# Kernel optimization log

Hardware: AMD Instinct MI355X
Metric: run time of the kernel (lower is better)

Reference implementation:

```python
import jax, jax.numpy as jnp
import numpy as np

DIM = 768
HEADS = 12
DIM_HEAD = DIM // HEADS
SEQ = 1024
BATCH = 16
DEPTH = 6
MAX_DEPTH = 12
ALPHA = 0.5


def _decomposed_kernel(n, depth, alpha, max_depth, inverse):
    # symmetric (inverse) matrix square root of the OU-process kernel matrix
    if depth == 0:
        return np.eye(n, dtype=np.float32)
    gamma = -0.5 * np.log(1.0 - alpha ** (2.0 * depth / max_depth))
    ar = np.arange(n, dtype=np.float64)
    K = np.exp(-gamma * np.abs(ar[:, None] - ar[None, :]))
    w, V = np.linalg.eigh(K)
    thr = w.max() * n * np.finfo(w.dtype).eps
    s = np.clip(w, thr, None)
    s = 1.0 / np.sqrt(s) if inverse else np.sqrt(s)
    return ((V * s[None, :]) @ V.T).astype(np.float32)


def _make_buffers():
    prev_inv = _decomposed_kernel(SEQ, DEPTH - 1, ALPHA, MAX_DEPTH, inverse=True)
    cur = _decomposed_kernel(SEQ, DEPTH, ALPHA, MAX_DEPTH, inverse=False)
    A = (cur @ prev_inv).astype(np.float32)
    mn = A.min()
    if mn <= 0:
        A = np.clip(A, abs(mn) + np.finfo(np.float32).eps, None)
    row_sum = A.sum(1)                      # (N,)
    B = np.log(A / row_sum)                 # broadcast over last axis (matches torch)
    d = row_sum.reshape(1, 1, SEQ, 1).astype(np.float32)
    return jnp.asarray(d), jnp.asarray(B[None, None]).astype(jnp.float32)


def setup_inputs() -> dict:
    key = jax.random.key(0)
    kx, kw = jax.random.split(key)
    x = jax.random.normal(kx, (BATCH, SEQ, DIM), dtype=jnp.float32)
    # module zeros the q block; use normal(std=dim^-0.5) everywhere for a non-degenerate test
    w_qkv = jax.random.normal(kw, (3 * DIM, DIM), dtype=jnp.float32) * (DIM ** -0.5)
    b_qkv = jnp.zeros((3 * DIM,), dtype=jnp.float32)
    d, b_bias = _make_buffers()
    return {"x": x, "w_qkv": w_qkv, "b_qkv": b_qkv, "d": d, "b_bias": b_bias}


def reference(x, w_qkv, b_qkv, d, b_bias):
    B, N, D = x.shape
    qkv = x @ w_qkv.T + b_qkv                                   # (B,N,3D)
    qkv = qkv.reshape(B, N, 3, HEADS, DIM_HEAD).transpose(2, 0, 3, 1, 4)
    q, k, v = qkv[0], qkv[1], qkv[2]                            # (B,H,N,dh)
    scale = DIM_HEAD ** -0.5
    scores = jnp.einsum("bhnd,bhmd->bhnm", q, k) * scale + b_bias
    attn = jax.nn.softmax(scores, axis=-1)
    out = d * jnp.einsum("bhnm,bhmd->bhnd", attn, v)            # post-softmax row scale
    return out.transpose(0, 2, 1, 3).reshape(B, N, D)
```

## Files before the change

kernel.cpp:

```cpp
#include <hip/hip_runtime.h>
#include <cstdint>
#include <cstddef>

typedef __attribute__((ext_vector_type(8))) short short8;
typedef __attribute__((ext_vector_type(4))) short short4_;
typedef __attribute__((ext_vector_type(4))) float f32x4;
typedef __attribute__((ext_vector_type(2))) unsigned int uint2_;

__device__ inline unsigned short bf16rne(float f) {
    uint32_t u = __builtin_bit_cast(uint32_t, f);
    u += 0x7fffu + ((u >> 16) & 1u);
    return (unsigned short)(u >> 16);
}

#define GLDS(g, l)                                                              \
    __builtin_amdgcn_global_load_lds(                                           \
        (const __attribute__((address_space(1))) void*)(g),                     \
        (__attribute__((address_space(3))) void*)(l), 16, 0, 0)

__global__ void cvt_kernel(const float* __restrict__ src,
                           unsigned short* __restrict__ dst, int n8) {
    int i = blockIdx.x * blockDim.x + threadIdx.x;
    if (i >= n8) return;
    const float4* s = (const float4*)src + (size_t)i * 2;
    float4 a = s[0], b = s[1];
    uint32_t w0 = bf16rne(a.x) | ((uint32_t)bf16rne(a.y) << 16);
    uint32_t w1 = bf16rne(a.z) | ((uint32_t)bf16rne(a.w) << 16);
    uint32_t w2 = bf16rne(b.x) | ((uint32_t)bf16rne(b.y) << 16);
    uint32_t w3 = bf16rne(b.z) | ((uint32_t)bf16rne(b.w) << 16);
    uint4 o; o.x = w0; o.y = w1; o.z = w2; o.w = w3;
    ((uint4*)dst)[i] = o;
}

__global__ __launch_bounds__(256) void qkv_gemm(
    const unsigned short* __restrict__ X, const unsigned short* __restrict__ W,
    const float* __restrict__ bqkv,
    unsigned short* __restrict__ qo, unsigned short* __restrict__ ko,
    unsigned short* __restrict__ vo)
{
    __shared__ unsigned short smem[16896];
    unsigned short* As = smem;
    unsigned short* Bs = smem + 8192;

    const int tid  = threadIdx.x;
    const int f    = blockIdx.x + gridDim.x * blockIdx.y;
    const int per  = (gridDim.x * gridDim.y) >> 3;
    const int wk   = (f & 7) * per + (f >> 3);
    const int m0   = (wk / 18) * 128;
    const int n0   = (wk % 18) * 128;
    const int wid  = tid >> 6;
    const int lane = tid & 63;
    const int m16  = lane & 15;
    const int quad = lane >> 4;
    const int wm   = wid >> 1, wn = wid & 1;

    f32x4 acc[4][4];
    #pragma unroll
    for (int i = 0; i < 4; i++)
        #pragma unroll
        for (int j = 0; j < 4; j++) acc[i][j] = (f32x4){0.f, 0.f, 0.f, 0.f};

    auto stage = [&](int buf, int k0) {
        #pragma unroll
        for (int rd = 0; rd < 2; ++rd) {
            int id = rd * 256 + tid;
            int row = id >> 2;
            int cs = (id & 3) ^ (row & 3);
            GLDS(X + (size_t)(m0 + row) * 768 + k0 + cs * 8, &As[buf * 4096 + id * 8]);
        }
        #pragma unroll
        for (int rd = 0; rd < 2; ++rd) {
            int id = rd * 256 + tid;
            int row = id >> 2;
            int cs = (id & 3) ^ (row & 3);
            GLDS(W + (size_t)(n0 + row) * 768 + k0 + cs * 8, &Bs[buf * 4096 + id * 8]);
        }
    };

    stage(0, 0);
    __syncthreads();

    const int csw = (quad ^ (m16 & 3)) * 8;
    for (int kt = 0; kt < 24; ++kt) {
        const int cur = kt & 1;
        if (kt < 23) stage(cur ^ 1, (kt + 1) * 32);

        short8 a[4], b[4];
        #pragma unroll
        for (int mb = 0; mb < 4; mb++)
            a[mb] = *(const short8*)&As[cur * 4096 + (wm * 64 + mb * 16 + m16) * 32 + csw];
        #pragma unroll
        for (int nb = 0; nb < 4; nb++)
            b[nb] = *(const short8*)&Bs[cur * 4096 + (wn * 64 + nb * 16 + m16) * 32 + csw];
        __builtin_amdgcn_s_setprio(1);
        #pragma unroll
        for (int mb = 0; mb < 4; mb++)
            #pragma unroll
            for (int nb = 0; nb < 4; nb++)
                acc[mb][nb] = __builtin_amdgcn_mfma_f32_16x16x32_bf16(
                    a[mb], b[nb], acc[mb][nb], 0, 0, 0);
        __builtin_amdgcn_s_setprio(0);
        __syncthreads();
    }

    float bias_n[4];
    #pragma unroll
    for (int nb = 0; nb < 4; nb++) bias_n[nb] = bqkv[n0 + wn * 64 + nb * 16 + m16];

    const int which = n0 / 768;
    const int hbase = (n0 % 768) / 64;
    const int bI  = m0 >> 10;
    const int ns0 = m0 & 1023;

    if (which == 2) {
        #pragma unroll
        for (int mb = 0; mb < 4; ++mb)
            #pragma unroll
            for (int nb = 0; nb < 4; ++nb) {
                int n  = wn * 64 + nb * 16 + m16;
                int hh = hbase + (n >> 6);
                int d  = n & 63;
                int pos = ns0 + wm * 64 + mb * 16 + quad * 4;
                short4_ v4;
                #pragma unroll
                for (int r = 0; r < 4; ++r)
                    v4[r] = (short)bf16rne(acc[mb][nb][r] + bias_n[nb]);
                *(short4_*)(vo + ((size_t)(bI * 12 + hh) * 64 + d) * 1024 + pos) = v4;
            }
        return;
    }

    const float qscale = (which == 0) ? 0.125f : 1.0f;
    #pragma unroll
    for (int mb = 0; mb < 4; mb++)
        #pragma unroll
        for (int nb = 0; nb < 4; nb++)
            #pragma unroll
            for (int r = 0; r < 4; r++) {
                float v = (acc[mb][nb][r] + bias_n[nb]) * qscale;
                smem[(wm * 64 + mb * 16 + quad * 4 + r) * 132 + wn * 64 + nb * 16 + m16] =
                    bf16rne(v);
            }
    __syncthreads();

    unsigned short* outp = (which == 0) ? qo : ko;
    #pragma unroll
    for (int rd = 0; rd < 8; ++rd) {
        int id = rd * 256 + tid;
        int row = id >> 4, c = id & 15;
        short4_ lo = *(const short4_*)&smem[row * 132 + c * 8];
        short4_ hi = *(const short4_*)&smem[row * 132 + c * 8 + 4];
        short8 v8 = __builtin_shufflevector(lo, hi, 0, 1, 2, 3, 4, 5, 6, 7);
        int h  = hbase + (c >> 3);
        int dc = (c & 7) * 8;
        unsigned short* dst =
            outp + ((size_t)(bI * 12 + h) * 1024 + ns0 + row) * 64 + dc;
        *(short8*)dst = v8;
    }
}

__global__ __launch_bounds__(512, 4) void attn_kernel(
    const unsigned short* __restrict__ Q, const unsigned short* __restrict__ K,
    const unsigned short* __restrict__ Vt, const float* __restrict__ bias,
    const float* __restrict__ dvec, float* __restrict__ out, int nbh8)
{
    __shared__ unsigned short Ks[2][4096];
    __shared__ unsigned short Vs[2][4096];

    const int tid  = threadIdx.x;
    const int wid  = tid >> 6;
    const int lane = tid & 63;
    const int m16  = lane & 15;
    const int quad = lane >> 4;

    const int f    = blockIdx.x;
    const int xcd  = f & 7;
    const int r_   = f >> 3;
    const int qt   = r_ & 7;
    const int bhl  = r_ >> 3;
    const int bh   = xcd * nbh8 + bhl;
    const int b = bh / 12, h = bh % 12;
    const int q0 = qt * 128;
    const int qrow = q0 + wid * 16 + m16;

    const unsigned short* Qb = Q  + (size_t)bh * 65536;
    const unsigned short* Kb = K  + (size_t)bh * 65536;
    const unsigned short* Vb = Vt + (size_t)bh * 65536;
    const float* brow = bias + (size_t)qrow * 1024 + quad * 4;

    int k_src, v_src;
    {
        int pos = tid >> 3, dbs = tid & 7;
        int db = dbs ^ (pos & 7);
        k_src = pos * 64 + db * 8;
        int pb = tid >> 6, d = tid & 63;
        v_src = d * 1024 + pb * 8;
    }

    short8 qf0 = *(const short8*)(Qb + (size_t)qrow * 64 + quad * 8);
    short8 qf1 = *(const short8*)(Qb + (size_t)qrow * 64 + 32 + quad * 8);

    f32x4 acc[4];
    #pragma unroll
    for (int nb = 0; nb < 4; nb++) acc[nb] = (f32x4){0.f, 0.f, 0.f, 0.f};
    float m_i = -3.0e38f, l_i = 0.f;
    const float L2E = 1.4426950408889634f;

    GLDS(Kb + k_src, &Ks[0][tid * 8]);
    GLDS(Vb + v_src, &Vs[0][tid * 8]);
    float4 bv[4];
    #pragma unroll
    for (int cb = 0; cb < 4; ++cb) bv[cb] = *(const float4*)(brow + cb * 16);
    __syncthreads();

    for (int kv = 0; kv < 16; ++kv) {
        const int cur = kv & 1;
        const int k0n = (kv + 1) * 64;

        f32x4 sc[4];
        #pragma unroll
        for (int cb = 0; cb < 4; ++cb) {
            sc[cb][0] = bv[cb].x;
            sc[cb][1] = bv[cb].y;
            sc[cb][2] = bv[cb].z;
            sc[cb][3] = bv[cb].w;
        }

        if (kv < 15) {
            GLDS(Kb + (size_t)k0n * 64 + k_src, &Ks[cur ^ 1][tid * 8]);
            GLDS(Vb + (size_t)k0n + v_src, &Vs[cur ^ 1][tid * 8]);
            #pragma unroll
            for (int cb = 0; cb < 4; ++cb)
                bv[cb] = *(const float4*)(brow + k0n + cb * 16);
        }

        __builtin_amdgcn_s_setprio(1);
        #pragma unroll
        for (int ks = 0; ks < 2; ++ks) {
            #pragma unroll
            for (int cb = 0; cb < 4; ++cb) {
                int pos = cb * 16 + m16;
                int slot = pos * 8 + ((ks * 4 + quad) ^ (m16 & 7));
                short8 a = *(const short8*)&Ks[cur][slot * 8];
                sc[cb] = __builtin_amdgcn_mfma_f32_16x16x32_bf16(
                    a, (ks == 0) ? qf0 : qf1, sc[cb], 0, 0, 0);
            }
        }
        __builtin_amdgcn_s_setprio(0);

        float mx = -3.0e38f;
        #pragma unroll
        for (int cb = 0; cb < 4; ++cb)
            mx = fmaxf(mx, fmaxf(fmaxf(sc[cb][0], sc[cb][1]), fmaxf(sc[cb][2], sc[cb][3])));
        mx = fmaxf(mx, __shfl_xor(mx, 16, 64));
        mx = fmaxf(mx, __shfl_xor(mx, 32, 64));

        if (!__all(mx <= m_i)) {
            float mnew = fmaxf(m_i, mx);
            float al = __builtin_amdgcn_exp2f((m_i - mnew) * L2E);
            m_i = mnew;
            l_i *= al;
            #pragma unroll
            for (int nb = 0; nb < 4; nb++) {
                acc[nb][0] *= al; acc[nb][1] *= al;
                acc[nb][2] *= al; acc[nb][3] *= al;
            }
        }
        const float nmL = -m_i * L2E;

        float rs = 0.f;
        short4_ pf[4];
        #pragma unroll
        for (int cb = 0; cb < 4; ++cb) {
            float p0 = __builtin_amdgcn_exp2f(__builtin_fmaf(sc[cb][0], L2E, nmL));
            float p1 = __builtin_amdgcn_exp2f(__builtin_fmaf(sc[cb][1], L2E, nmL));
            float p2 = __builtin_amdgcn_exp2f(__builtin_fmaf(sc[cb][2], L2E, nmL));
            float p3 = __builtin_amdgcn_exp2f(__builtin_fmaf(sc[cb][3], L2E, nmL));
            rs += (p0 + p1) + (p2 + p3);
            uint2_ pd;
            pd[0] = __builtin_amdgcn_perm(__builtin_bit_cast(uint32_t, p1),
                                          __builtin_bit_cast(uint32_t, p0), 0x07060302u);
            pd[1] = __builtin_amdgcn_perm(__builtin_bit_cast(uint32_t, p3),
                                          __builtin_bit_cast(uint32_t, p2), 0x07060302u);
            pf[cb] = __builtin_bit_cast(short4_, pd);
        }
        rs += __shfl_xor(rs, 16, 64);
        rs += __shfl_xor(rs, 32, 64);
        l_i += rs;

        __builtin_amdgcn_s_setprio(1);
        #pragma unroll
        for (int ks = 0; ks < 4; ++ks) {
            #pragma unroll
            for (int nb = 0; nb < 4; ++nb) {
                int slot = (ks * 2 + (quad >> 1)) * 64 + nb * 16 + m16;
                short4_ av = *(const short4_*)&Vs[cur][slot * 8 + (quad & 1) * 4];
                acc[nb] = __builtin_amdgcn_mfma_f32_16x16x16bf16_1k(av, pf[ks], acc[nb], 0, 0, 0);
            }
        }
        __builtin_amdgcn_s_setprio(0);

        __syncthreads();
    }

    float scl = dvec[qrow] / l_i;
    #pragma unroll
    for (int nb = 0; nb < 4; ++nb) {
        float4 o;
        o.x = acc[nb][0] * scl; o.y = acc[nb][1] * scl;
        o.z = acc[nb][2] * scl; o.w = acc[nb][3] * scl;
        *(float4*)(out + ((size_t)b * 1024 + qrow) * 768 + h * 64 + nb * 16 + quad * 4) = o;
    }
}

extern "C" void kernel_launch(void* const* d_in, const int* in_sizes, int n_in,
                              void* d_out, int out_size, void* d_ws, size_t ws_size,
                              hipStream_t stream) {
    const float* x     = (const float*)d_in[0];
    const float* w     = (const float*)d_in[1];
    const float* bqkv  = (const float*)d_in[2];
    const float* dvec  = (const float*)d_in[3];
    const float* bbias = (const float*)d_in[4];
    float* out = (float*)d_out;

    char* ws = (char*)d_ws;
    unsigned short* wb = (unsigned short*)ws;
    unsigned short* xb = (unsigned short*)((char*)d_out + 25165824);

    cvt_kernel<<<6144, 256, 0, stream>>>(x, xb, 1572864);
    cvt_kernel<<<864, 256, 0, stream>>>(w, wb, 221184);

    const size_t NEED_FULL = 3538944ull + 3ull * 25165824ull;
    if (ws_size >= NEED_FULL) {
        unsigned short* qb = (unsigned short*)(ws + 3538944);
        unsigned short* kb = qb + 12582912;
        unsigned short* vb = kb + 12582912;
        qkv_gemm<<<dim3(18, 128), 256, 0, stream>>>(xb, wb, bqkv, qb, kb, vb);
        attn_kernel<<<1536, 512, 0, stream>>>(qb, kb, vb, bbias, dvec, out, 24);
    } else {
        unsigned short* qb = (unsigned short*)(ws + 3538944);
        unsigned short* kb = qb + 3145728;
        unsigned short* vb = kb + 3145728;
        for (int c = 0; c < 4; ++c) {
            const unsigned short* xc = xb + (size_t)c * 3145728;
            qkv_gemm<<<dim3(18, 32), 256, 0, stream>>>(xc, wb, bqkv, qb, kb, vb);
            attn_kernel<<<384, 512, 0, stream>>>(
                qb, kb, vb, bbias, dvec, out + (size_t)c * 3145728, 6);
        }
    }
}
```

Baseline: 317.3 us.

## Enlarge QKV GEMM tiles to 256x256 with deeper K pipeline and transposed Q

The QKV projection GEMM moves from 128x128 tiles with 256 threads to 256x256 tiles with 512 threads and a K-step of 64. Staging is double-buffered with explicit vmcnt waits and raw barriers, so the next global-to-LDS load overlaps compute. The Q output is now written transposed (d-major) the same way as V, which makes the attention kernel gather Q with strided scalar loads. The aim is more data reuse and fewer blocks. The cost is a 128KB LDS footprint, more accumulator registers, and uncoalesced Q loads in attention.

Result: no change. 314.7 us (-0.8%).

```diff
diff --git a/kernel.cpp b/kernel.cpp
--- a/kernel.cpp
+++ b/kernel.cpp
@@ -32,75 +32,89 @@
     ((uint4*)dst)[i] = o;
 }
 
-__global__ __launch_bounds__(256) void qkv_gemm(
+__global__ __launch_bounds__(512, 2) void qkv_gemm(
     const unsigned short* __restrict__ X, const unsigned short* __restrict__ W,
     const float* __restrict__ bqkv,
     unsigned short* __restrict__ qo, unsigned short* __restrict__ ko,
     unsigned short* __restrict__ vo)
 {
-    __shared__ unsigned short smem[16896];
+    __shared__ unsigned short smem[65536];
     unsigned short* As = smem;
-    unsigned short* Bs = smem + 8192;
+    unsigned short* Bs = smem + 32768;
 
     const int tid  = threadIdx.x;
-    const int f    = blockIdx.x + gridDim.x * blockIdx.y;
-    const int per  = (gridDim.x * gridDim.y) >> 3;
+    const int f    = blockIdx.x;
+    const int per  = gridDim.x >> 3;
     const int wk   = (f & 7) * per + (f >> 3);
-    const int m0   = (wk / 18) * 128;
-    const int n0   = (wk % 18) * 128;
+    const int m0   = (wk / 9) * 256;
+    const int n0   = (wk % 9) * 256;
     const int wid  = tid >> 6;
     const int lane = tid & 63;
     const int m16  = lane & 15;
     const int quad = lane >> 4;
-    const int wm   = wid >> 1, wn = wid & 1;
-
-    f32x4 acc[4][4];
-    #pragma unroll
-    for (int i = 0; i < 4; i++)
+    const int wm   = wid >> 2;
+    const int wn   = wid & 3;
+
+    f32x4 acc[8][4];
+    #pragma unroll
+    for (int i = 0; i < 8; i++)
         #pragma unroll
         for (int j = 0; j < 4; j++) acc[i][j] = (f32x4){0.f, 0.f, 0.f, 0.f};
 
     auto stage = [&](int buf, int k0) {
         #pragma unroll
-        for (int rd = 0; rd < 2; ++rd) {
-            int id = rd * 256 + tid;
-            int row = id >> 2;
-            int cs = (id & 3) ^ (row & 3);
-            GLDS(X + (size_t)(m0 + row) * 768 + k0 + cs * 8, &As[buf * 4096 + id * 8]);
-        }
-        #pragma unroll
-        for (int rd = 0; rd < 2; ++rd) {
-            int id = rd * 256 + tid;
-            int row = id >> 2;
-            int cs = (id & 3) ^ (row & 3);
-            GLDS(W + (size_t)(n0 + row) * 768 + k0 + cs * 8, &Bs[buf * 4096 + id * 8]);
+        for (int rd = 0; rd < 4; ++rd) {
+            int id = rd * 512 + tid;
+            int row = id >> 3;
+            int cs = (id & 7) ^ (row & 7);
+            GLDS(X + (size_t)(m0 + row) * 768 + k0 + cs * 8,
+                 &As[buf * 16384 + id * 8]);
+        }
+        #pragma unroll
+        for (int rd = 0; rd < 4; ++rd) {
+            int id = rd * 512 + tid;
+            int row = id >> 3;
+            int cs = (id & 7) ^ (row & 7);
+            GLDS(W + (size_t)(n0 + row) * 768 + k0 + cs * 8,
+                 &Bs[buf * 16384 + id * 8]);
         }
     };
 
     stage(0, 0);
-    __syncthreads();
-
-    const int csw = (quad ^ (m16 & 3)) * 8;
-    for (int kt = 0; kt < 24; ++kt) {
-        const int cur = kt & 1;
-        if (kt < 23) stage(cur ^ 1, (kt + 1) * 32);
-
-        short8 a[4], b[4];
-        #pragma unroll
-        for (int mb = 0; mb < 4; mb++)
-            a[mb] = *(const short8*)&As[cur * 4096 + (wm * 64 + mb * 16 + m16) * 32 + csw];
-        #pragma unroll
-        for (int nb = 0; nb < 4; nb++)
-            b[nb] = *(const short8*)&Bs[cur * 4096 + (wn * 64 + nb * 16 + m16) * 32 + csw];
+    stage(1, 64);
+
+    const int arow0 = wm * 128 + m16;
+    const int brow0 = wn * 64 + m16;
+    const int swz   = m16 & 7;
+
+    for (int t = 0; t < 12; ++t) {
+        const int cur = t & 1;
+        if (t == 11) asm volatile("s_waitcnt vmcnt(0)" ::: "memory");
+        else         asm volatile("s_waitcnt vmcnt(8)" ::: "memory");
+        __builtin_amdgcn_s_barrier();
+
         __builtin_amdgcn_s_setprio(1);
         #pragma unroll
-        for (int mb = 0; mb < 4; mb++)
+        for (int ks = 0; ks < 2; ++ks) {
+            const int ch = ((ks * 4 + quad) ^ swz) * 8;
+            short8 b[4];
             #pragma unroll
             for (int nb = 0; nb < 4; nb++)
-                acc[mb][nb] = __builtin_amdgcn_mfma_f32_16x16x32_bf16(
-                    a[mb], b[nb], acc[mb][nb], 0, 0, 0);
+                b[nb] = *(const short8*)&Bs[cur * 16384 + (brow0 + nb * 16) * 64 + ch];
+            #pragma unroll
+            for (int mb = 0; mb < 8; mb++) {
+                short8 a = *(const short8*)&As[cur * 16384 + (arow0 + mb * 16) * 64 + ch];
+                #pragma unroll
+                for (int nb = 0; nb < 4; nb++)
+                    acc[mb][nb] = __builtin_amdgcn_mfma_f32_16x16x32_bf16(
+                        a, b[nb], acc[mb][nb], 0, 0, 0);
+            }
+        }
         __builtin_amdgcn_s_setprio(0);
-        __syncthreads();
+
+        __builtin_amdgcn_s_barrier();
+        asm volatile("" ::: "memory");
+        if (t < 10) stage(cur, (t + 2) * 64);
     }
 
     float bias_n[4];
@@ -108,54 +122,59 @@
     for (int nb = 0; nb < 4; nb++) bias_n[nb] = bqkv[n0 + wn * 64 + nb * 16 + m16];
 
     const int which = n0 / 768;
-    const int hbase = (n0 % 768) / 64;
+    const int hbase = (n0 % 768) >> 6;
     const int bI  = m0 >> 10;
     const int ns0 = m0 & 1023;
 
-    if (which == 2) {
-        #pragma unroll
-        for (int mb = 0; mb < 4; ++mb)
+    if (which != 1) {
+        unsigned short* outp = (which == 0) ? qo : vo;
+        const float scl = (which == 0) ? 0.125f : 1.0f;
+        const int h = hbase + wn;
+        #pragma unroll
+        for (int mb = 0; mb < 8; ++mb)
             #pragma unroll
             for (int nb = 0; nb < 4; ++nb) {
-                int n  = wn * 64 + nb * 16 + m16;
-                int hh = hbase + (n >> 6);
-                int d  = n & 63;
-                int pos = ns0 + wm * 64 + mb * 16 + quad * 4;
+                int d   = nb * 16 + m16;
+                int pos = ns0 + wm * 128 + mb * 16 + quad * 4;
                 short4_ v4;
                 #pragma unroll
                 for (int r = 0; r < 4; ++r)
-                    v4[r] = (short)bf16rne(acc[mb][nb][r] + bias_n[nb]);
-                *(short4_*)(vo + ((size_t)(bI * 12 + hh) * 64 + d) * 1024 + pos) = v4;
+                    v4[r] = (short)bf16rne((acc[mb][nb][r] + bias_n[nb]) * scl);
+                *(short4_*)(outp + ((size_t)(bI * 12 + h) * 64 + d) * 1024 + pos) = v4;
             }
         return;
     }
 
-    const float qscale = (which == 0) ? 0.125f : 1.0f;
-    #pragma unroll
-    for (int mb = 0; mb < 4; mb++)
-        #pragma unroll
-        for (int nb = 0; nb < 4; nb++)
-            #pragma unroll
-            for (int r = 0; r < 4; r++) {
-                float v = (acc[mb][nb][r] + bias_n[nb]) * qscale;
-                smem[(wm * 64 + mb * 16 + quad * 4 + r) * 132 + wn * 64 + nb * 16 + m16] =
-                    bf16rne(v);
-            }
-    __syncthreads();
-
-    unsigned short* outp = (which == 0) ? qo : ko;
-    #pragma unroll
-    for (int rd = 0; rd < 8; ++rd) {
-        int id = rd * 256 + tid;
-        int row = id >> 4, c = id & 15;
-        short4_ lo = *(const short4_*)&smem[row * 132 + c * 8];
-        short4_ hi = *(const short4_*)&smem[row * 132 + c * 8 + 4];
-        short8 v8 = __builtin_shufflevector(lo, hi, 0, 1, 2, 3, 4, 5, 6, 7);
-        int h  = hbase + (c >> 3);
-        int dc = (c & 7) * 8;
-        unsigned short* dst =
-            outp + ((size_t)(bI * 12 + h) * 1024 + ns0 + row) * 64 + dc;
-        *(short8*)dst = v8;
+    #pragma unroll
+    for (int pass = 0; pass < 2; ++pass) {
+        __syncthreads();
+        if ((wn >> 1) == pass) {
+            const int colb = (wn & 1) * 64;
+            #pragma unroll
+            for (int mb = 0; mb < 8; mb++)
+                #pragma unroll
+                for (int nb = 0; nb < 4; nb++)
+                    #pragma unroll
+                    for (int r = 0; r < 4; r++) {
+                        float v = acc[mb][nb][r] + bias_n[nb];
+                        smem[(wm * 128 + mb * 16 + quad * 4 + r) * 132 +
+                             colb + nb * 16 + m16] = bf16rne(v);
+                    }
+        }
+        __syncthreads();
+        #pragma unroll
+        for (int rd = 0; rd < 8; ++rd) {
+            int id = rd * 512 + tid;
+            int row = id >> 4, c = id & 15;
+            short4_ lo = *(const short4_*)&smem[row * 132 + c * 8];
+            short4_ hi = *(const short4_*)&smem[row * 132 + c * 8 + 4];
+            short8 v8 = __builtin_shufflevector(lo, hi, 0, 1, 2, 3, 4, 5, 6, 7);
+            int h  = hbase + pass * 2 + (c >> 3);
+            int dc = (c & 7) * 8;
+            unsigned short* dst =
+                ko + ((size_t)(bI * 12 + h) * 1024 + ns0 + row) * 64 + dc;
+            *(short8*)dst = v8;
+        }
     }
 }
 
@@ -197,8 +216,12 @@
         v_src = d * 1024 + pb * 8;
     }
 
-    short8 qf0 = *(const short8*)(Qb + (size_t)qrow * 64 + quad * 8);
-    short8 qf1 = *(const short8*)(Qb + (size_t)qrow * 64 + 32 + quad * 8);
+    short8 qf0, qf1;
+    #pragma unroll
+    for (int j = 0; j < 8; ++j) {
+        qf0[j] = (short)Qb[(size_t)(quad * 8 + j) * 1024 + qrow];
+        qf1[j] = (short)Qb[(size_t)(32 + quad * 8 + j) * 1024 + qrow];
+    }
 
     f32x4 acc[4];
     #pragma unroll
@@ -335,7 +358,7 @@
         unsigned short* qb = (unsigned short*)(ws + 3538944);
         unsigned short* kb = qb + 12582912;
         unsigned short* vb = kb + 12582912;
-        qkv_gemm<<<dim3(18, 128), 256, 0, stream>>>(xb, wb, bqkv, qb, kb, vb);
+        qkv_gemm<<<576, 512, 0, stream>>>(xb, wb, bqkv, qb, kb, vb);
         attn_kernel<<<1536, 512, 0, stream>>>(qb, kb, vb, bbias, dvec, out, 24);
     } else {
         unsigned short* qb = (unsigned short*)(ws + 3538944);
@@ -343,7 +366,7 @@
         unsigned short* vb = kb + 3145728;
         for (int c = 0; c < 4; ++c) {
             const unsigned short* xc = xb + (size_t)c * 3145728;
-            qkv_gemm<<<dim3(18, 32), 256, 0, stream>>>(xc, wb, bqkv, qb, kb, vb);
+            qkv_gemm<<<144, 512, 0, stream>>>(xc, wb, bqkv, qb, kb, vb);
             attn_kernel<<<384, 512, 0, stream>>>(
                 qb, kb, vb, bbias, dvec, out + (size_t)c * 3145728, 6);
         }
```
